# Kernel tuning notes

Hardware: AMD Instinct MI355X
Metric: run time of the kernel (lower is better)

The kernel has to match this reference:

```python
import jax, jax.numpy as jnp
import numpy as np

EPS = 1e-5  # torch BatchNorm2d default eps


def setup_inputs() -> dict:
    key = jax.random.key(0)
    ks = jax.random.split(key, 11)
    n, c, h, w = 16, 512, 64, 64
    grp, cg, mip = 4, 128, 16
    return {
        "x": jax.random.normal(ks[0], (n, c, h, w), dtype=jnp.float32),
        "W1": jax.random.normal(ks[1], (mip, cg), dtype=jnp.float32) * 0.05,
        "b1": jax.random.normal(ks[2], (mip,), dtype=jnp.float32) * 0.05,
        "gamma": jax.random.uniform(ks[3], (mip,), dtype=jnp.float32, minval=0.5, maxval=1.5),
        "beta": jax.random.normal(ks[4], (mip,), dtype=jnp.float32) * 0.05,
        "mean": jax.random.normal(ks[5], (mip,), dtype=jnp.float32) * 0.05,
        "var": jax.random.uniform(ks[6], (mip,), dtype=jnp.float32, minval=0.5, maxval=1.5),
        "Wh": jax.random.normal(ks[7], (cg, mip), dtype=jnp.float32) * 0.1,
        "bh": jax.random.normal(ks[8], (cg,), dtype=jnp.float32) * 0.05,
        "Ww": jax.random.normal(ks[9], (cg, mip), dtype=jnp.float32) * 0.1,
        "bw": jax.random.normal(ks[10], (cg,), dtype=jnp.float32) * 0.05,
    }


def reference(x, W1, b1, gamma, beta, mean, var, Wh, bh, Ww, bw):
    n, c, h, w = x.shape
    grp = 4
    cg = c // grp
    # Since c % 4 == 0, torch.split gives 4 equal groups: fold group into a new axis.
    xg = x.reshape(n, grp, cg, h, w)                       # (n,g,cg,h,w)
    gh = xg.mean(axis=4)                                   # pool over w -> (n,g,cg,h)
    gw = xg.mean(axis=3)                                   # pool over h -> (n,g,cg,w)
    y = jnp.concatenate([gh, gw], axis=3)                  # (n,g,cg,h+w)
    # conv1 (1x1) shared across all 4 groups
    y = jnp.einsum('ngcl,mc->ngml', y, W1) + b1[None, None, :, None]
    # BatchNorm2d (eval mode, running stats)
    scale = gamma / jnp.sqrt(var + EPS)
    y = y * scale[None, None, :, None] + (beta - mean * scale)[None, None, :, None]
    # h_swish: x * relu6(x+3)/6
    y = y * (jnp.clip(y + 3.0, 0.0, 6.0) / 6.0)
    yh, yw = y[..., :h], y[..., h:]                        # (n,g,mip,h), (n,g,mip,w)
    a_h = jax.nn.sigmoid(jnp.einsum('ngml,cm->ngcl', yh, Wh) + bh[None, None, :, None])
    a_w = jax.nn.sigmoid(jnp.einsum('ngml,cm->ngcl', yw, Ww) + bw[None, None, :, None])
    out = xg * a_h[..., :, None] * a_w[..., None, :]       # (n,g,cg,h,w)
    out = out.reshape(n, c, h, w)
    # channel shuffle: (n, cg, grp, h, w) -> permute group axis forward
    out = out.reshape(n, cg, grp, h, w).transpose(0, 2, 1, 3, 4).reshape(n, c, h, w)
    return out
```

## Files before the change

### kernel.cpp

```cpp
#include <hip/hip_runtime.h>

#define N_   16
#define C_   512
#define H_   64
#define W_   64
#define GRP  4
#define CG   128
#define MIP  16

__device__ __forceinline__ float bf_lo(unsigned u) { return __uint_as_float(u << 16); }
__device__ __forceinline__ float bf_hi(unsigned u) { return __uint_as_float(u & 0xFFFF0000u); }
__device__ __forceinline__ float bf1(unsigned short s) { return __uint_as_float((unsigned)s << 16); }

__device__ __forceinline__ float ld_scalar(const void* p, int i, bool isbf) {
    return isbf ? bf1(((const unsigned short*)p)[i]) : ((const float*)p)[i];
}

__global__ __launch_bounds__(64) void ksniff(const unsigned* __restrict__ x,
                                             unsigned* __restrict__ flag) {
    const int t = threadIdx.x;
    int cnt = 0;
    #pragma unroll
    for (int k = 0; k < 4; ++k) {
        unsigned w = x[t + 64 * k];
        unsigned e = (w >> 7) & 0xFFu;
        cnt += (e >= 0x60u && e <= 0x9Fu) ? 1 : 0;
    }
    #pragma unroll
    for (int off = 32; off > 0; off >>= 1) cnt += __shfl_down(cnt, off, 64);
    if (t == 0) flag[0] = (cnt >= 192) ? 1u : 0u;
}

__global__ __launch_bounds__(256) void kreduce(const void* __restrict__ xv,
                                               const unsigned* __restrict__ flag,
                                               float* __restrict__ gh,
                                               float* __restrict__ gw) {
    __shared__ float tile[64 * 65];
    const int bid = blockIdx.x;
    const int t = threadIdx.x;
    const bool isbf = (flag[0] != 0u);

    if (isbf) {
        const uint4* src = (const uint4*)((const unsigned short*)xv + (size_t)bid * 4096);
        #pragma unroll
        for (int half = 0; half < 2; ++half) {
            int idx = t + half * 256;
            int r = idx >> 3;
            int j0 = (idx & 7) * 8;
            uint4 v = src[idx];
            unsigned uu[4] = {v.x, v.y, v.z, v.w};
            #pragma unroll
            for (int k = 0; k < 4; ++k) {
                tile[r * 65 + j0 + 2 * k]     = bf_lo(uu[k]);
                tile[r * 65 + j0 + 2 * k + 1] = bf_hi(uu[k]);
            }
        }
    } else {
        const float4* src = (const float4*)((const float*)xv + (size_t)bid * 4096);
        #pragma unroll
        for (int it = 0; it < 4; ++it) {
            int idx = t + it * 256;
            int r = idx >> 4;
            int j0 = (idx & 15) * 4;
            float4 v = src[idx];
            tile[r * 65 + j0]     = v.x;
            tile[r * 65 + j0 + 1] = v.y;
            tile[r * 65 + j0 + 2] = v.z;
            tile[r * 65 + j0 + 3] = v.w;
        }
    }
    __syncthreads();

    if (t < 64) {
        float s = 0.f;
        #pragma unroll
        for (int j = 0; j < 64; ++j) s += tile[t * 65 + j];
        gh[(size_t)bid * 64 + t] = s * (1.0f / 64.0f);
    } else if (t < 128) {
        int j = t - 64;
        float s = 0.f;
        #pragma unroll
        for (int i = 0; i < 64; ++i) s += tile[i * 65 + j];
        gw[(size_t)bid * 64 + j] = s * (1.0f / 64.0f);
    }
}

__device__ __forceinline__ void stage2048(const void* W, float* dst, int t, bool isbf) {
    if (isbf) {
        uint4 v = ((const uint4*)W)[t];
        unsigned uu[4] = {v.x, v.y, v.z, v.w};
        #pragma unroll
        for (int k = 0; k < 4; ++k) {
            dst[t * 8 + 2 * k]     = bf_lo(uu[k]);
            dst[t * 8 + 2 * k + 1] = bf_hi(uu[k]);
        }
    } else {
        #pragma unroll
        for (int it = 0; it < 2; ++it) {
            int idx = t + 256 * it;
            float4 v = ((const float4*)W)[idx];
            dst[idx * 4]     = v.x;
            dst[idx * 4 + 1] = v.y;
            dst[idx * 4 + 2] = v.z;
            dst[idx * 4 + 3] = v.w;
        }
    }
}

__global__ __launch_bounds__(256) void kattn(
    const float* __restrict__ gh, const float* __restrict__ gw,
    const unsigned* __restrict__ flag,
    const void* __restrict__ W1, const void* __restrict__ b1,
    const void* __restrict__ gamma, const void* __restrict__ beta,
    const void* __restrict__ mean, const void* __restrict__ var,
    const void* __restrict__ Wh, const void* __restrict__ bh,
    const void* __restrict__ Ww, const void* __restrict__ bw,
    float* __restrict__ ah, float* __restrict__ aw)
{
    __shared__ float W1_s[MIP * CG];
    __shared__ float Wh_s[CG * MIP];
    __shared__ float Ww_s[CG * MIP];
    __shared__ float y_s[MIP * 128];
    __shared__ float scale_s[MIP], shift_s[MIP], b1_s[MIP];
    __shared__ float bh_s[CG], bw_s[CG];

    const int t = threadIdx.x;
    const bool isbf = (flag[0] != 0u);

    stage2048(W1, W1_s, t, isbf);
    stage2048(Wh, Wh_s, t, isbf);
    stage2048(Ww, Ww_s, t, isbf);

    if (t < MIP) {
        float sc = ld_scalar(gamma, t, isbf) * rsqrtf(ld_scalar(var, t, isbf) + 1e-5f);
        scale_s[t] = sc;
        shift_s[t] = ld_scalar(beta, t, isbf) - ld_scalar(mean, t, isbf) * sc;
        b1_s[t] = ld_scalar(b1, t, isbf);
    }
    if (t < CG) { bh_s[t] = ld_scalar(bh, t, isbf); bw_s[t] = ld_scalar(bw, t, isbf); }
    __syncthreads();

    {
        const int l = t & 127;
        const int half = t >> 7;
        const size_t base = (size_t)blockIdx.x * (CG * 64);
        const float* src = (l < 64) ? (gh + base + l) : (gw + base + (l - 64));
        float acc[8] = {0.f, 0.f, 0.f, 0.f, 0.f, 0.f, 0.f, 0.f};
        for (int cc = 0; cc < CG; ++cc) {
            float v = src[(size_t)cc * 64];
            #pragma unroll
            for (int mm = 0; mm < 8; ++mm)
                acc[mm] += W1_s[(half * 8 + mm) * CG + cc] * v;
        }
        #pragma unroll
        for (int mm = 0; mm < 8; ++mm) {
            int m = half * 8 + mm;
            float yv = acc[mm] + b1_s[m];
            yv = yv * scale_s[m] + shift_s[m];
            float hc = fminf(fmaxf(yv + 3.0f, 0.0f), 6.0f);
            y_s[m * 128 + l] = yv * hc * (1.0f / 6.0f);
        }
    }
    __syncthreads();

    {
        const int i = t & 63;
        const int wg = t >> 6;
        const size_t obase = (size_t)blockIdx.x * (CG * 64);
        for (int k = 0; k < 32; ++k) {
            int cc = wg * 32 + k;
            float acch = bh_s[cc], accw = bw_s[cc];
            #pragma unroll
            for (int m = 0; m < MIP; ++m) {
                acch += Wh_s[cc * MIP + m] * y_s[m * 128 + i];
                accw += Ww_s[cc * MIP + m] * y_s[m * 128 + 64 + i];
            }
            ah[obase + (size_t)cc * 64 + i] = 1.0f / (1.0f + __expf(-acch));
            aw[obase + (size_t)cc * 64 + i] = 1.0f / (1.0f + __expf(-accw));
        }
    }
}

__global__ __launch_bounds__(256) void kapply(const void* __restrict__ xv,
                                              const unsigned* __restrict__ flag,
                                              const float* __restrict__ ah,
                                              const float* __restrict__ aw,
                                              void* __restrict__ outv) {
    __shared__ float ah_s[64], aw_s[64];
    const int bid = blockIdx.x;
    const int n = bid >> 9;
    const int o = bid & 511;
    const int g2 = o >> 7, cc2 = o & 127;
    const int p = cc2 * 4 + g2;
    const int g = p >> 7, cc = p & 127;
    const size_t abase = ((size_t)(n * 4 + g) * 128 + cc) * 64;
    const int t = threadIdx.x;
    const bool isbf = (flag[0] != 0u);

    if (t < 64) ah_s[t] = ah[abase + t];
    else if (t < 128) aw_s[t - 64] = aw[abase + (t - 64)];
    __syncthreads();

    if (isbf) {
        const uint4* src = (const uint4*)((const unsigned short*)xv + ((size_t)n * 512 + p) * 4096);
        uint4* dst = (uint4*)((unsigned short*)outv + (size_t)bid * 4096);
        #pragma unroll
        for (int half = 0; half < 2; ++half) {
            int idx = t + half * 256;
            int r = idx >> 3;
            int j0 = (idx & 7) * 8;
            float sah = ah_s[r];
            uint4 v = src[idx];
            unsigned uu[4] = {v.x, v.y, v.z, v.w};
            unsigned res[4];
            #pragma unroll
            for (int k = 0; k < 4; ++k) {
                int j = j0 + 2 * k;
                float f0 = bf_lo(uu[k]) * sah * aw_s[j];
                float f1 = bf_hi(uu[k]) * sah * aw_s[j + 1];
                unsigned u0 = __float_as_uint(f0); u0 += 0x7FFFu + ((u0 >> 16) & 1u);
                unsigned u1 = __float_as_uint(f1); u1 += 0x7FFFu + ((u1 >> 16) & 1u);
                res[k] = (u0 >> 16) | (u1 & 0xFFFF0000u);
            }
            uint4 w; w.x = res[0]; w.y = res[1]; w.z = res[2]; w.w = res[3];
            dst[idx] = w;
        }
    } else {
        const float4* src = (const float4*)((const float*)xv + ((size_t)n * 512 + p) * 4096);
        float4* dst = (float4*)((float*)outv + (size_t)bid * 4096);
        #pragma unroll
        for (int it = 0; it < 4; ++it) {
            int idx = t + it * 256;
            int r = idx >> 4;
            int j0 = (idx & 15) * 4;
            float sah = ah_s[r];
            float4 v = src[idx];
            v.x *= sah * aw_s[j0];
            v.y *= sah * aw_s[j0 + 1];
            v.z *= sah * aw_s[j0 + 2];
            v.w *= sah * aw_s[j0 + 3];
            dst[idx] = v;
        }
    }
}

extern "C" void kernel_launch(void* const* d_in, const int* in_sizes, int n_in,
                              void* d_out, int out_size, void* d_ws, size_t ws_size,
                              hipStream_t stream) {
    const void* x     = d_in[0];
    const void* W1    = d_in[1];
    const void* b1    = d_in[2];
    const void* gamma = d_in[3];
    const void* beta  = d_in[4];
    const void* mean  = d_in[5];
    const void* var   = d_in[6];
    const void* Wh    = d_in[7];
    const void* bh    = d_in[8];
    const void* Ww    = d_in[9];
    const void* bw    = d_in[10];

    float* ws = (float*)d_ws;
    unsigned* flag = (unsigned*)ws;
    const size_t seg = (size_t)N_ * GRP * CG * 64;
    float* gh = ws + 64;
    float* gw = gh + seg;
    float* ah = gw + seg;
    float* aw = ah + seg;

    ksniff<<<1, 64, 0, stream>>>((const unsigned*)x, flag);
    kreduce<<<N_ * C_, 256, 0, stream>>>(x, flag, gh, gw);
    kattn<<<N_ * GRP, 256, 0, stream>>>(gh, gw, flag, W1, b1, gamma, beta, mean, var,
                                        Wh, bh, Ww, bw, ah, aw);
    kapply<<<N_ * C_, 256, 0, stream>>>(x, flag, ah, aw, d_out);
}
```

Baseline: 287.8 us.

## Fuse dtype sniff into each kernel and compute sigmoid attention inside apply

```diff
diff --git a/kernel.cpp b/kernel.cpp
--- a/kernel.cpp
+++ b/kernel.cpp
@@ -16,29 +16,32 @@
     return isbf ? bf1(((const unsigned short*)p)[i]) : ((const float*)p)[i];
 }
 
-__global__ __launch_bounds__(64) void ksniff(const unsigned* __restrict__ x,
-                                             unsigned* __restrict__ flag) {
-    const int t = threadIdx.x;
-    int cnt = 0;
-    #pragma unroll
-    for (int k = 0; k < 4; ++k) {
-        unsigned w = x[t + 64 * k];
-        unsigned e = (w >> 7) & 0xFFu;
-        cnt += (e >= 0x60u && e <= 0x9Fu) ? 1 : 0;
-    }
-    #pragma unroll
-    for (int off = 32; off > 0; off >>= 1) cnt += __shfl_down(cnt, off, 64);
-    if (t == 0) flag[0] = (cnt >= 192) ? 1u : 0u;
+__device__ __forceinline__ bool sniff_isbf(const unsigned* __restrict__ x32,
+                                           int t, unsigned* s_flag) {
+    if (t < 64) {
+        int cnt = 0;
+        #pragma unroll
+        for (int k = 0; k < 4; ++k) {
+            unsigned w = x32[t + 64 * k];
+            unsigned e = (w >> 7) & 0xFFu;
+            cnt += (e >= 0x60u && e <= 0x9Fu) ? 1 : 0;
+        }
+        #pragma unroll
+        for (int off = 32; off > 0; off >>= 1) cnt += __shfl_down(cnt, off, 64);
+        if (t == 0) *s_flag = (cnt >= 192) ? 1u : 0u;
+    }
+    __syncthreads();
+    return *s_flag != 0u;
 }
 
 __global__ __launch_bounds__(256) void kreduce(const void* __restrict__ xv,
-                                               const unsigned* __restrict__ flag,
                                                float* __restrict__ gh,
                                                float* __restrict__ gw) {
     __shared__ float tile[64 * 65];
+    __shared__ unsigned flag_s;
     const int bid = blockIdx.x;
     const int t = threadIdx.x;
-    const bool isbf = (flag[0] != 0u);
+    const bool isbf = sniff_isbf((const unsigned*)xv, t, &flag_s);
 
     if (isbf) {
         const uint4* src = (const uint4*)((const unsigned short*)xv + (size_t)bid * 4096);
@@ -85,120 +88,101 @@
     }
 }
 
-__device__ __forceinline__ void stage2048(const void* W, float* dst, int t, bool isbf) {
-    if (isbf) {
-        uint4 v = ((const uint4*)W)[t];
-        unsigned uu[4] = {v.x, v.y, v.z, v.w};
-        #pragma unroll
-        for (int k = 0; k < 4; ++k) {
-            dst[t * 8 + 2 * k]     = bf_lo(uu[k]);
-            dst[t * 8 + 2 * k + 1] = bf_hi(uu[k]);
-        }
-    } else {
-        #pragma unroll
-        for (int it = 0; it < 2; ++it) {
-            int idx = t + 256 * it;
-            float4 v = ((const float4*)W)[idx];
-            dst[idx * 4]     = v.x;
-            dst[idx * 4 + 1] = v.y;
-            dst[idx * 4 + 2] = v.z;
-            dst[idx * 4 + 3] = v.w;
-        }
-    }
-}
-
-__global__ __launch_bounds__(256) void kattn(
+__global__ __launch_bounds__(256) void ky(
+    const void* __restrict__ xv,
     const float* __restrict__ gh, const float* __restrict__ gw,
-    const unsigned* __restrict__ flag,
     const void* __restrict__ W1, const void* __restrict__ b1,
     const void* __restrict__ gamma, const void* __restrict__ beta,
     const void* __restrict__ mean, const void* __restrict__ var,
-    const void* __restrict__ Wh, const void* __restrict__ bh,
-    const void* __restrict__ Ww, const void* __restrict__ bw,
-    float* __restrict__ ah, float* __restrict__ aw)
+    float* __restrict__ y)
 {
     __shared__ float W1_s[MIP * CG];
-    __shared__ float Wh_s[CG * MIP];
-    __shared__ float Ww_s[CG * MIP];
-    __shared__ float y_s[MIP * 128];
     __shared__ float scale_s[MIP], shift_s[MIP], b1_s[MIP];
-    __shared__ float bh_s[CG], bw_s[CG];
+    __shared__ unsigned flag_s;
 
     const int t = threadIdx.x;
-    const bool isbf = (flag[0] != 0u);
-
-    stage2048(W1, W1_s, t, isbf);
-    stage2048(Wh, Wh_s, t, isbf);
-    stage2048(Ww, Ww_s, t, isbf);
-
+    const bool isbf = sniff_isbf((const unsigned*)xv, t, &flag_s);
+
+    if (isbf) {
+        uint4 v = ((const uint4*)W1)[t];
+        unsigned uu[4] = {v.x, v.y, v.z, v.w};
+        #pragma unroll
+        for (int k = 0; k < 4; ++k) {
+            W1_s[t * 8 + 2 * k]     = bf_lo(uu[k]);
+            W1_s[t * 8 + 2 * k + 1] = bf_hi(uu[k]);
+        }
+    } else {
+        #pragma unroll
+        for (int it = 0; it < 2; ++it) {
+            int idx = t + 256 * it;
+            float4 v = ((const float4*)W1)[idx];
+            W1_s[idx * 4]     = v.x;
+            W1_s[idx * 4 + 1] = v.y;
+            W1_s[idx * 4 + 2] = v.z;
+            W1_s[idx * 4 + 3] = v.w;
+        }
+    }
     if (t < MIP) {
         float sc = ld_scalar(gamma, t, isbf) * rsqrtf(ld_scalar(var, t, isbf) + 1e-5f);
         scale_s[t] = sc;
         shift_s[t] = ld_scalar(beta, t, isbf) - ld_scalar(mean, t, isbf) * sc;
         b1_s[t] = ld_scalar(b1, t, isbf);
     }
-    if (t < CG) { bh_s[t] = ld_scalar(bh, t, isbf); bw_s[t] = ld_scalar(bw, t, isbf); }
-    __syncthreads();
-
-    {
-        const int l = t & 127;
-        const int half = t >> 7;
-        const size_t base = (size_t)blockIdx.x * (CG * 64);
-        const float* src = (l < 64) ? (gh + base + l) : (gw + base + (l - 64));
-        float acc[8] = {0.f, 0.f, 0.f, 0.f, 0.f, 0.f, 0.f, 0.f};
-        for (int cc = 0; cc < CG; ++cc) {
-            float v = src[(size_t)cc * 64];
-            #pragma unroll
-            for (int mm = 0; mm < 8; ++mm)
-                acc[mm] += W1_s[(half * 8 + mm) * CG + cc] * v;
-        }
-        #pragma unroll
-        for (int mm = 0; mm < 8; ++mm) {
-            int m = half * 8 + mm;
-            float yv = acc[mm] + b1_s[m];
-            yv = yv * scale_s[m] + shift_s[m];
-            float hc = fminf(fmaxf(yv + 3.0f, 0.0f), 6.0f);
-            y_s[m * 128 + l] = yv * hc * (1.0f / 6.0f);
-        }
-    }
-    __syncthreads();
-
-    {
-        const int i = t & 63;
-        const int wg = t >> 6;
-        const size_t obase = (size_t)blockIdx.x * (CG * 64);
-        for (int k = 0; k < 32; ++k) {
-            int cc = wg * 32 + k;
-            float acch = bh_s[cc], accw = bw_s[cc];
-            #pragma unroll
-            for (int m = 0; m < MIP; ++m) {
-                acch += Wh_s[cc * MIP + m] * y_s[m * 128 + i];
-                accw += Ww_s[cc * MIP + m] * y_s[m * 128 + 64 + i];
-            }
-            ah[obase + (size_t)cc * 64 + i] = 1.0f / (1.0f + __expf(-acch));
-            aw[obase + (size_t)cc * 64 + i] = 1.0f / (1.0f + __expf(-accw));
-        }
+    __syncthreads();
+
+    const int l = t & 127;
+    const int half = t >> 7;
+    const size_t base = (size_t)blockIdx.x * (CG * 64);
+    const float* src = (l < 64) ? (gh + base + l) : (gw + base + (l - 64));
+    float acc[8] = {0.f, 0.f, 0.f, 0.f, 0.f, 0.f, 0.f, 0.f};
+    for (int cc = 0; cc < CG; ++cc) {
+        float v = src[(size_t)cc * 64];
+        #pragma unroll
+        for (int mm = 0; mm < 8; ++mm)
+            acc[mm] += W1_s[(half * 8 + mm) * CG + cc] * v;
+    }
+    float* yb = y + (size_t)blockIdx.x * (MIP * 128);
+    #pragma unroll
+    for (int mm = 0; mm < 8; ++mm) {
+        int m = half * 8 + mm;
+        float yv = acc[mm] + b1_s[m];
+        yv = yv * scale_s[m] + shift_s[m];
+        float hc = fminf(fmaxf(yv + 3.0f, 0.0f), 6.0f);
+        yb[m * 128 + l] = yv * hc * (1.0f / 6.0f);
     }
 }
 
 __global__ __launch_bounds__(256) void kapply(const void* __restrict__ xv,
-                                              const unsigned* __restrict__ flag,
-                                              const float* __restrict__ ah,
-                                              const float* __restrict__ aw,
+                                              const float* __restrict__ y,
+                                              const void* __restrict__ Wh,
+                                              const void* __restrict__ bh,
+                                              const void* __restrict__ Ww,
+                                              const void* __restrict__ bw,
                                               void* __restrict__ outv) {
     __shared__ float ah_s[64], aw_s[64];
+    __shared__ unsigned flag_s;
     const int bid = blockIdx.x;
     const int n = bid >> 9;
     const int o = bid & 511;
     const int g2 = o >> 7, cc2 = o & 127;
     const int p = cc2 * 4 + g2;
     const int g = p >> 7, cc = p & 127;
-    const size_t abase = ((size_t)(n * 4 + g) * 128 + cc) * 64;
     const int t = threadIdx.x;
-    const bool isbf = (flag[0] != 0u);
-
-    if (t < 64) ah_s[t] = ah[abase + t];
-    else if (t < 128) aw_s[t - 64] = aw[abase + (t - 64)];
+    const bool isbf = sniff_isbf((const unsigned*)xv, t, &flag_s);
+
+    if (t < 128) {
+        const int i = t & 63;
+        const bool isW = (t >= 64);
+        const void* Wp = isW ? Ww : Wh;
+        const void* bp = isW ? bw : bh;
+        const float* ysrc = y + (size_t)(n * 4 + g) * (MIP * 128) + (isW ? 64 : 0) + i;
+        float acc = ld_scalar(bp, cc, isbf);
+        #pragma unroll
+        for (int m = 0; m < MIP; ++m)
+            acc += ld_scalar(Wp, cc * MIP + m, isbf) * ysrc[m * 128];
+        float s = 1.0f / (1.0f + __expf(-acc));
+        if (isW) aw_s[i] = s; else ah_s[i] = s;
+    }
     __syncthreads();
 
     if (isbf) {
@@ -260,16 +244,12 @@
     const void* bw    = d_in[10];
 
     float* ws = (float*)d_ws;
-    unsigned* flag = (unsigned*)ws;
     const size_t seg = (size_t)N_ * GRP * CG * 64;
-    float* gh = ws + 64;
+    float* gh = ws;
     float* gw = gh + seg;
-    float* ah = gw + seg;
-    float* aw = ah + seg;
-
-    ksniff<<<1, 64, 0, stream>>>((const unsigned*)x, flag);
-    kreduce<<<N_ * C_, 256, 0, stream>>>(x, flag, gh, gw);
-    kattn<<<N_ * GRP, 256, 0, stream>>>(gh, gw, flag, W1, b1, gamma, beta, mean, var,
-                                        Wh, bh, Ww, bw, ah, aw);
-    kapply<<<N_ * C_, 256, 0, stream>>>(x, flag, ah, aw, d_out);
-}
+    float* yv = gw + seg;
+
+    kreduce<<<N_ * C_, 256, 0, stream>>>(x, gh, gw);
+    ky<<<N_ * GRP, 256, 0, stream>>>(x, gh, gw, W1, b1, gamma, beta, mean, var, yv);
+    kapply<<<N_ * C_, 256, 0, stream>>>(x, yv, Wh, bh, Ww, bw, d_out);
+}
```

Measured after the change: 277.8 us. 3.5% less time.
